# Kernel tuning notes

Hardware: AMD Instinct MI355X
Metric: run time of the kernel (lower is better)

## Reference

```python
import jax, jax.numpy as jnp
import numpy as np

N = 40000      # nodes
D = 64         # nnodefeatures
DEG = 32       # avg in-degree
E = N * DEG    # edges
G = 200        # graphs in batch
ATT = 64       # attention_size
HID = 128      # cls_hidden_dim
NCLS = 6
NLAYERS = 3


def setup_inputs() -> dict:
    key = jax.random.key(0)
    ks = jax.random.split(key, 8)
    s = 0.05
    x = jax.random.normal(ks[0], (N, D), dtype=jnp.float32)
    row = jax.random.randint(ks[1], (E,), 0, N, dtype=jnp.int32)
    # every node appears as a target exactly DEG times -> no zero degrees
    col = jnp.repeat(jnp.arange(N, dtype=jnp.int32), DEG)
    edge_index = jnp.stack([row, col])
    batch = jnp.repeat(jnp.arange(G, dtype=jnp.int32), N // G)
    W_lin = jax.random.normal(ks[2], (D, D), jnp.float32) * s
    b_lin = jnp.zeros((D,), jnp.float32)
    W_att = jax.random.normal(ks[3], (ATT, 2 * D), jnp.float32) * s
    a_vec = jnp.ones((ATT, 1), jnp.float32)  # torch.ones init
    W1 = jax.random.normal(ks[4], (HID, D), jnp.float32) * s
    b1 = jnp.zeros((HID,), jnp.float32)
    W2 = jax.random.normal(ks[5], (NCLS, HID), jnp.float32) * s
    b2 = jnp.zeros((NCLS,), jnp.float32)
    return dict(x=x, W_lin=W_lin, b_lin=b_lin, W_att=W_att, a_vec=a_vec,
                W1=W1, b1=b1, W2=W2, b2=b2,
                edge_index=edge_index, batch=batch, n_graphs=G)


def _gnn_layer(x, row, col, W_lin, b_lin, W_att, a_vec):
    n = x.shape[0]
    deg = jnp.sqrt(jax.ops.segment_sum(jnp.ones_like(col, dtype=x.dtype), col, num_segments=n))
    deg = jnp.where(jnp.isinf(deg), jnp.zeros_like(deg), deg)  # deg[deg==inf]=0
    norm = deg[row] * deg[col]                                  # [E]
    x_j = x[row]                                                # [E, D] gather source
    x_i = x[col]                                                # [E, D] gather target
    att_in = jnp.concatenate([x_j, x_i], axis=-1)               # [E, 2D]
    score = jnp.exp((att_in @ W_att.T) @ a_vec)                 # [E, 1]
    att_norm = jax.ops.segment_sum(score, col, num_segments=n)  # [N, 1] (scatter by edge_index[1])
    att = score / att_norm[row]                                 # gathered at edge_index[0] (faithful)
    m = ((x_j * att) @ W_lin.T + b_lin) / norm[:, None]         # [E, D]
    out = jax.ops.segment_sum(m, col, num_segments=n)           # aggregate by target
    return jax.nn.selu(out)


def reference(x, W_lin, b_lin, W_att, a_vec, W1, b1, W2, b2, edge_index, batch, n_graphs):
    row, col = edge_index[0], edge_index[1]
    # Faithful to original: the loop re-applies the layer to the ORIGINAL x each time
    for _ in range(NLAYERS):
        h = _gnn_layer(x, row, col, W_lin, b_lin, W_att, a_vec)
    sums = jax.ops.segment_sum(h, batch, num_segments=n_graphs)
    counts = jax.ops.segment_sum(jnp.ones((x.shape[0],), x.dtype), batch, num_segments=n_graphs)
    pooled = sums / counts[:, None]                              # global_mean_pool
    hcls = jax.nn.selu(pooled @ W1.T + b1)
    logits = hcls @ W2.T + b2
    return jax.nn.softmax(logits, axis=-1)
```

## Files before the change

kernel.cpp:

```cpp
#include <hip/hip_runtime.h>
#include <hip/hip_bf16.h>

#define N_NODES 40000
#define D_FEAT 64
#define DEG 32
#define E_EDGES (N_NODES * DEG)
#define G_GRAPHS 200
#define NPG 200
#define ATT_SZ 64
#define HID 128
#define NCLS 6
#define XS 68

__device__ __forceinline__ float selu_f(float x) {
    const float scale = 1.0507009873554805f;
    const float alpha = 1.6732632423543772f;
    return scale * (x > 0.f ? x : alpha * (__expf(x) - 1.f));
}

__global__ void k_watt(const float* __restrict__ Watt,
                       const float* __restrict__ avec,
                       float* __restrict__ w) {
    int j = threadIdx.x;
    float s = 0.f;
    for (int k = 0; k < ATT_SZ; ++k)
        s += avec[k] * Watt[k * 128 + j];
    w[j] = s;
}

__global__ __launch_bounds__(256) void k_node(const float* __restrict__ x,
                                              const float* __restrict__ Wlin,
                                              const float* __restrict__ w,
                                              float* __restrict__ P,
                                              float* __restrict__ Q,
                                              float* __restrict__ y) {
    __shared__ float xs[64 * XS];
    __shared__ float wsT[64 * XS];
    __shared__ float ws_w[128];
    int tid = threadIdx.x;
    int n0 = blockIdx.x * 64;

    const float4* x4 = (const float4*)(x + (size_t)n0 * 64);
    const float4* W4 = (const float4*)Wlin;
#pragma unroll
    for (int s = 0; s < 4; ++s) {
        int idx = tid + s * 256;
        int r = idx >> 4, kk = idx & 15;
        float4 v = x4[idx];
        *(float4*)&xs[r * XS + kk * 4] = v;
        float4 wv = W4[idx];
        wsT[(kk * 4 + 0) * XS + r] = wv.x;
        wsT[(kk * 4 + 1) * XS + r] = wv.y;
        wsT[(kk * 4 + 2) * XS + r] = wv.z;
        wsT[(kk * 4 + 3) * XS + r] = wv.w;
    }
    if (tid < 128) ws_w[tid] = w[tid];
    __syncthreads();

    {
        int node = tid >> 2, part = tid & 3;
        float s1 = 0.f, s2 = 0.f;
#pragma unroll
        for (int i = 0; i < 16; ++i) {
            int k = part * 16 + i;
            float xv = xs[node * XS + k];
            s1 += xv * ws_w[k];
            s2 += xv * ws_w[64 + k];
        }
        s1 += __shfl_xor(s1, 1, 64); s1 += __shfl_xor(s1, 2, 64);
        s2 += __shfl_xor(s2, 1, 64); s2 += __shfl_xor(s2, 2, 64);
        if (part == 0) { P[n0 + node] = __expf(s1); Q[n0 + node] = __expf(s2); }
    }

    int tm = tid >> 4, tf = tid & 15;
    int f0 = tf * 4;
    float4 acc[4];
#pragma unroll
    for (int i = 0; i < 4; ++i) acc[i] = make_float4(0.f, 0.f, 0.f, 0.f);
#pragma unroll
    for (int kk = 0; kk < 16; ++kk) {
        float4 w0 = *(const float4*)&wsT[(kk * 4 + 0) * XS + f0];
        float4 w1 = *(const float4*)&wsT[(kk * 4 + 1) * XS + f0];
        float4 w2 = *(const float4*)&wsT[(kk * 4 + 2) * XS + f0];
        float4 w3 = *(const float4*)&wsT[(kk * 4 + 3) * XS + f0];
#pragma unroll
        for (int i = 0; i < 4; ++i) {
            float4 xv = *(const float4*)&xs[(tm + 16 * i) * XS + kk * 4];
            acc[i].x += xv.x * w0.x + xv.y * w1.x + xv.z * w2.x + xv.w * w3.x;
            acc[i].y += xv.x * w0.y + xv.y * w1.y + xv.z * w2.y + xv.w * w3.y;
            acc[i].z += xv.x * w0.z + xv.y * w1.z + xv.z * w2.z + xv.w * w3.z;
            acc[i].w += xv.x * w0.w + xv.y * w1.w + xv.z * w2.w + xv.w * w3.w;
        }
    }
#pragma unroll
    for (int i = 0; i < 4; ++i)
        *(float4*)&y[(size_t)(n0 + tm + 16 * i) * 64 + f0] = acc[i];
}

__global__ __launch_bounds__(256) void k_edges(const int* __restrict__ row,
                                               const float* __restrict__ P,
                                               const float* __restrict__ Q,
                                               float* __restrict__ V) {
    int e = blockIdx.x * 256 + threadIdx.x;
    float p = P[row[e]];
#pragma unroll
    for (int off = 16; off; off >>= 1)
        p += __shfl_xor(p, off, 32);
    if ((threadIdx.x & 31) == 0) {
        int n = e >> 5;
        V[n] = P[n] / (Q[n] * p);
    }
}

__global__ __launch_bounds__(256) void k_agg(const int* __restrict__ row,
                                             const float* __restrict__ V,
                                             const float* __restrict__ Q,
                                             const float* __restrict__ y,
                                             const float* __restrict__ blin,
                                             float* __restrict__ pool) {
    int tid = threadIdx.x;
    int wave = tid >> 6, lane = tid & 63;
    int half = lane >> 5, fl = lane & 31;
    int n0 = __builtin_amdgcn_readfirstlane((blockIdx.x * 4 + wave) * 8);
    float2 bl = ((const float2*)blin)[fl];
    float2 pacc = make_float2(0.f, 0.f);
#pragma unroll 1
    for (int nn = 0; nn < 8; ++nn) {
        int n = n0 + nn;
        const int* rp = row + n * 32;
        float2 acc = make_float2(0.f, 0.f);
#pragma unroll
        for (int s = 0; s < 16; ++s) {
            int re = rp[2 * s];
            int ro = rp[2 * s + 1];
            float ve = V[re];
            float vo = V[ro];
            int r = half ? ro : re;
            float v = half ? vo : ve;
            float2 t = ((const float2*)(y + (size_t)r * 64))[fl];
            acc.x += v * t.x;
            acc.y += v * t.y;
        }
        acc.x += __shfl_xor(acc.x, 32, 64);
        acc.y += __shfl_xor(acc.y, 32, 64);
        float qn = Q[n];
        pacc.x += selu_f(qn * acc.x * (1.f / 32.f) + bl.x);
        pacc.y += selu_f(qn * acc.y * (1.f / 32.f) + bl.y);
    }
    int g = n0 / NPG;
    if (half == 0) {
        atomicAdd(&pool[g * 64 + 2 * fl], pacc.x);
        atomicAdd(&pool[g * 64 + 2 * fl + 1], pacc.y);
    }
}

__global__ __launch_bounds__(128) void k_cls(const float* __restrict__ pool,
                                             const float* __restrict__ W1,
                                             const float* __restrict__ b1,
                                             const float* __restrict__ W2,
                                             const float* __restrict__ b2,
                                             float* __restrict__ out) {
    __shared__ float ps[64];
    __shared__ float hc[HID];
    __shared__ float lg[NCLS];
    int t = threadIdx.x, g = blockIdx.x;
    if (t < 64) ps[t] = pool[g * 64 + t] * (1.f / NPG);
    __syncthreads();
    float s = b1[t];
    for (int k = 0; k < 64; ++k)
        s += W1[t * 64 + k] * ps[k];
    hc[t] = selu_f(s);
    __syncthreads();
    if (t < NCLS) {
        float l = b2[t];
        for (int k = 0; k < HID; ++k)
            l += W2[t * 128 + k] * hc[k];
        lg[t] = l;
    }
    __syncthreads();
    if (t == 0) {
        float m = lg[0];
        for (int c = 1; c < NCLS; ++c) m = fmaxf(m, lg[c]);
        float ex[NCLS], sum = 0.f;
        for (int c = 0; c < NCLS; ++c) { ex[c] = __expf(lg[c] - m); sum += ex[c]; }
        for (int c = 0; c < NCLS; ++c) out[g * NCLS + c] = ex[c] / sum;
    }
}

extern "C" void kernel_launch(void* const* d_in, const int* in_sizes, int n_in,
                              void* d_out, int out_size, void* d_ws, size_t ws_size,
                              hipStream_t stream) {
    const float* x    = (const float*)d_in[0];
    const float* Wlin = (const float*)d_in[1];
    const float* blin = (const float*)d_in[2];
    const float* Watt = (const float*)d_in[3];
    const float* avec = (const float*)d_in[4];
    const float* W1   = (const float*)d_in[5];
    const float* b1   = (const float*)d_in[6];
    const float* W2   = (const float*)d_in[7];
    const float* b2   = (const float*)d_in[8];
    const int* eidx = (const int*)d_in[9];
    const int* row  = eidx;
    float* out = (float*)d_out;

    float* w    = (float*)d_ws;
    float* P    = w + 128;
    float* Q    = P + N_NODES;
    float* V    = Q + N_NODES;
    float* pool = V + N_NODES;
    float* y    = pool + G_GRAPHS * 64;

    hipMemsetAsync(pool, 0, G_GRAPHS * 64 * sizeof(float), stream);

    k_watt<<<1, 128, 0, stream>>>(Watt, avec, w);
    k_node<<<N_NODES / 64, 256, 0, stream>>>(x, Wlin, w, P, Q, y);
    k_edges<<<E_EDGES / 256, 256, 0, stream>>>(row, P, Q, V);
    k_agg<<<N_NODES / 32, 256, 0, stream>>>(row, V, Q, y, blin, pool);
    k_cls<<<G_GRAPHS, 128, 0, stream>>>(pool, W1, b1, W2, b2, out);
}
```

Baseline: 159.7 us.

## Store projected features as bf16, fold watt and memset into node kernel

The per-node projected features y are now stored as packed bf16 pairs, which halves the bytes gathered in the edge aggregation kernel. The separate attention-vector kernel and the pool memset are folded into k_node, removing a launch and a memset. The W_lin tile is kept untransposed with padding 69 and the inner product is restructured. The bf16 storage lowers the precision of aggregated messages, and every block now recomputes the 128-wide attention vector.

```diff
diff --git a/kernel.cpp b/kernel.cpp
--- a/kernel.cpp
+++ b/kernel.cpp
@@ -1,5 +1,6 @@
 #include <hip/hip_runtime.h>
 #include <hip/hip_bf16.h>
+#include <stdint.h>
 
 #define N_NODES 40000
 #define D_FEAT 64
@@ -10,7 +11,7 @@
 #define ATT_SZ 64
 #define HID 128
 #define NCLS 6
-#define XS 68
+#define XS 69
 
 __device__ __forceinline__ float selu_f(float x) {
     const float scale = 1.0507009873554805f;
@@ -18,27 +19,25 @@
     return scale * (x > 0.f ? x : alpha * (__expf(x) - 1.f));
 }
 
-__global__ void k_watt(const float* __restrict__ Watt,
-                       const float* __restrict__ avec,
-                       float* __restrict__ w) {
-    int j = threadIdx.x;
-    float s = 0.f;
-    for (int k = 0; k < ATT_SZ; ++k)
-        s += avec[k] * Watt[k * 128 + j];
-    w[j] = s;
+__device__ __forceinline__ uint32_t f2bf(float f) {
+    uint32_t u = __builtin_bit_cast(uint32_t, f);
+    return (u + 0x7fffu + ((u >> 16) & 1u)) >> 16;
 }
 
 __global__ __launch_bounds__(256) void k_node(const float* __restrict__ x,
                                               const float* __restrict__ Wlin,
-                                              const float* __restrict__ w,
+                                              const float* __restrict__ Watt,
+                                              const float* __restrict__ avec,
                                               float* __restrict__ P,
                                               float* __restrict__ Q,
-                                              float* __restrict__ y) {
+                                              uint32_t* __restrict__ yb,
+                                              float* __restrict__ pool) {
     __shared__ float xs[64 * XS];
-    __shared__ float wsT[64 * XS];
+    __shared__ float ws[64 * XS];
     __shared__ float ws_w[128];
     int tid = threadIdx.x;
     int n0 = blockIdx.x * 64;
+    if (blockIdx.x < 50) pool[blockIdx.x * 256 + tid] = 0.f;
 
     const float4* x4 = (const float4*)(x + (size_t)n0 * 64);
     const float4* W4 = (const float4*)Wlin;
@@ -46,15 +45,15 @@
     for (int s = 0; s < 4; ++s) {
         int idx = tid + s * 256;
         int r = idx >> 4, kk = idx & 15;
-        float4 v = x4[idx];
-        *(float4*)&xs[r * XS + kk * 4] = v;
-        float4 wv = W4[idx];
-        wsT[(kk * 4 + 0) * XS + r] = wv.x;
-        wsT[(kk * 4 + 1) * XS + r] = wv.y;
-        wsT[(kk * 4 + 2) * XS + r] = wv.z;
-        wsT[(kk * 4 + 3) * XS + r] = wv.w;
-    }
-    if (tid < 128) ws_w[tid] = w[tid];
+        *(float4*)&xs[r * XS + kk * 4] = x4[idx];
+        *(float4*)&ws[r * XS + kk * 4] = W4[idx];
+    }
+    if (tid < 128) {
+        float s = 0.f;
+        for (int k = 0; k < ATT_SZ; ++k)
+            s += avec[k] * Watt[k * 128 + tid];
+        ws_w[tid] = s;
+    }
     __syncthreads();
 
     {
@@ -73,28 +72,32 @@
     }
 
     int tm = tid >> 4, tf = tid & 15;
-    int f0 = tf * 4;
-    float4 acc[4];
-#pragma unroll
-    for (int i = 0; i < 4; ++i) acc[i] = make_float4(0.f, 0.f, 0.f, 0.f);
+    float acc[4][4];
+#pragma unroll
+    for (int i = 0; i < 4; ++i)
+#pragma unroll
+        for (int j = 0; j < 4; ++j) acc[i][j] = 0.f;
 #pragma unroll
     for (int kk = 0; kk < 16; ++kk) {
-        float4 w0 = *(const float4*)&wsT[(kk * 4 + 0) * XS + f0];
-        float4 w1 = *(const float4*)&wsT[(kk * 4 + 1) * XS + f0];
-        float4 w2 = *(const float4*)&wsT[(kk * 4 + 2) * XS + f0];
-        float4 w3 = *(const float4*)&wsT[(kk * 4 + 3) * XS + f0];
-#pragma unroll
-        for (int i = 0; i < 4; ++i) {
-            float4 xv = *(const float4*)&xs[(tm + 16 * i) * XS + kk * 4];
-            acc[i].x += xv.x * w0.x + xv.y * w1.x + xv.z * w2.x + xv.w * w3.x;
-            acc[i].y += xv.x * w0.y + xv.y * w1.y + xv.z * w2.y + xv.w * w3.y;
-            acc[i].z += xv.x * w0.z + xv.y * w1.z + xv.z * w2.z + xv.w * w3.z;
-            acc[i].w += xv.x * w0.w + xv.y * w1.w + xv.z * w2.w + xv.w * w3.w;
-        }
-    }
-#pragma unroll
-    for (int i = 0; i < 4; ++i)
-        *(float4*)&y[(size_t)(n0 + tm + 16 * i) * 64 + f0] = acc[i];
+        float4 xv[4], wv[4];
+#pragma unroll
+        for (int i = 0; i < 4; ++i) xv[i] = *(const float4*)&xs[(tm + 16 * i) * XS + kk * 4];
+#pragma unroll
+        for (int j = 0; j < 4; ++j) wv[j] = *(const float4*)&ws[(4 * tf + j) * XS + kk * 4];
+#pragma unroll
+        for (int i = 0; i < 4; ++i)
+#pragma unroll
+            for (int j = 0; j < 4; ++j)
+                acc[i][j] += xv[i].x * wv[j].x + xv[i].y * wv[j].y
+                           + xv[i].z * wv[j].z + xv[i].w * wv[j].w;
+    }
+#pragma unroll
+    for (int i = 0; i < 4; ++i) {
+        int m = n0 + tm + 16 * i;
+        uint32_t p0 = f2bf(acc[i][0]) | (f2bf(acc[i][1]) << 16);
+        uint32_t p1 = f2bf(acc[i][2]) | (f2bf(acc[i][3]) << 16);
+        *(uint2*)&yb[(size_t)m * 32 + tf * 2] = make_uint2(p0, p1);
+    }
 }
 
 __global__ __launch_bounds__(256) void k_edges(const int* __restrict__ row,
@@ -115,7 +118,7 @@
 __global__ __launch_bounds__(256) void k_agg(const int* __restrict__ row,
                                              const float* __restrict__ V,
                                              const float* __restrict__ Q,
-                                             const float* __restrict__ y,
+                                             const uint32_t* __restrict__ yb,
                                              const float* __restrict__ blin,
                                              float* __restrict__ pool) {
     int tid = threadIdx.x;
@@ -137,15 +140,17 @@
             float vo = V[ro];
             int r = half ? ro : re;
             float v = half ? vo : ve;
-            float2 t = ((const float2*)(y + (size_t)r * 64))[fl];
-            acc.x += v * t.x;
-            acc.y += v * t.y;
+            uint32_t u = yb[(size_t)r * 32 + fl];
+            float flo = __builtin_bit_cast(float, u << 16);
+            float fhi = __builtin_bit_cast(float, u & 0xffff0000u);
+            acc.x += v * flo;
+            acc.y += v * fhi;
         }
         acc.x += __shfl_xor(acc.x, 32, 64);
         acc.y += __shfl_xor(acc.y, 32, 64);
-        float qn = Q[n];
-        pacc.x += selu_f(qn * acc.x * (1.f / 32.f) + bl.x);
-        pacc.y += selu_f(qn * acc.y * (1.f / 32.f) + bl.y);
+        float qn = Q[n] * (1.f / 32.f);
+        pacc.x += selu_f(qn * acc.x + bl.x);
+        pacc.y += selu_f(qn * acc.y + bl.y);
     }
     int g = n0 / NPG;
     if (half == 0) {
@@ -203,18 +208,14 @@
     const int* row  = eidx;
     float* out = (float*)d_out;
 
-    float* w    = (float*)d_ws;
-    float* P    = w + 128;
+    float* P    = (float*)d_ws;
     float* Q    = P + N_NODES;
     float* V    = Q + N_NODES;
     float* pool = V + N_NODES;
-    float* y    = pool + G_GRAPHS * 64;
-
-    hipMemsetAsync(pool, 0, G_GRAPHS * 64 * sizeof(float), stream);
-
-    k_watt<<<1, 128, 0, stream>>>(Watt, avec, w);
-    k_node<<<N_NODES / 64, 256, 0, stream>>>(x, Wlin, w, P, Q, y);
+    uint32_t* yb = (uint32_t*)(pool + G_GRAPHS * 64);
+
+    k_node<<<N_NODES / 64, 256, 0, stream>>>(x, Wlin, Watt, avec, P, Q, yb, pool);
     k_edges<<<E_EDGES / 256, 256, 0, stream>>>(row, P, Q, V);
-    k_agg<<<N_NODES / 32, 256, 0, stream>>>(row, V, Q, y, blin, pool);
+    k_agg<<<N_NODES / 32, 256, 0, stream>>>(row, V, Q, yb, blin, pool);
     k_cls<<<G_GRAPHS, 128, 0, stream>>>(pool, W1, b1, W2, b2, out);
 }
```

Result: faster. 150.8 us (-5.6%).
